# Kernel optimization log

Measured on AMD Instinct MI355X. Metric: run time of the kernel, lower is better.

Reference implementation:

```python
import jax, jax.numpy as jnp
import numpy as np

NEG_SLOPE = 0.2
NEG_INF = -1e9


def _gat_branch(x, src, dst, edge_type, t, W, a_src, a_dst, b):
    """Single-head PyG GATConv restricted (by masking) to edges with edge_type == t,
    with self-loops added (PyG default add_self_loops=True)."""
    N = x.shape[0]
    h = x @ W                                   # [N, out_dim]
    s = h @ a_src                               # [N] source attention term
    d = h @ a_dst                               # [N] destination attention term
    # real edges (masked by type)
    e_edge = jax.nn.leaky_relu(s[src] + d[dst], NEG_SLOPE)
    e_edge = jnp.where(edge_type == t, e_edge, NEG_INF)
    # self-loop edges i -> i
    e_self = jax.nn.leaky_relu(s + d, NEG_SLOPE)
    dst_all = jnp.concatenate([dst, jnp.arange(N)])          # [E+N]
    e_all = jnp.concatenate([e_edge, e_self])                 # [E+N]
    # softmax over incoming edges per destination node (segment softmax)
    m = jax.ops.segment_max(e_all, dst_all, num_segments=N)
    p = jnp.exp(e_all - m[dst_all])
    denom = jax.ops.segment_sum(p, dst_all, num_segments=N)
    alpha = p / denom[dst_all]                                 # [E+N]
    msg = jnp.concatenate([h[src], h], axis=0) * alpha[:, None]
    return jax.ops.segment_sum(msg, dst_all, num_segments=N) + b


def setup_inputs() -> dict:
    key = jax.random.key(0)
    ks = jax.random.split(key, 12)
    N, E, in_dim, out_dim = 100000, 1000000, 64, 64
    glorot = (6.0 / (in_dim + out_dim)) ** 0.5
    att = (6.0 / (1 + out_dim)) ** 0.5
    return {
        "x": jax.random.normal(ks[0], (N, in_dim), dtype=jnp.float32),
        "edge_index": jax.random.randint(ks[1], (2, E), 0, N),
        "edge_type": jax.random.randint(ks[2], (E,), 0, 2),
        "W_login": jax.random.uniform(ks[3], (in_dim, out_dim), jnp.float32, -glorot, glorot),
        "a_src_login": jax.random.uniform(ks[4], (out_dim,), jnp.float32, -att, att),
        "a_dst_login": jax.random.uniform(ks[5], (out_dim,), jnp.float32, -att, att),
        "b_login": jnp.zeros((out_dim,), jnp.float32),
        "W_exec": jax.random.uniform(ks[6], (in_dim, out_dim), jnp.float32, -glorot, glorot),
        "a_src_exec": jax.random.uniform(ks[7], (out_dim,), jnp.float32, -att, att),
        "a_dst_exec": jax.random.uniform(ks[8], (out_dim,), jnp.float32, -att, att),
        "b_exec": jnp.zeros((out_dim,), jnp.float32),
    }


def reference(x, edge_index, edge_type, W_login, a_src_login, a_dst_login, b_login,
              W_exec, a_src_exec, a_dst_exec, b_exec):
    src, dst = edge_index[0], edge_index[1]
    out = _gat_branch(x, src, dst, edge_type, 0, W_login, a_src_login, a_dst_login, b_login)
    out = out + _gat_branch(x, src, dst, edge_type, 1, W_exec, a_src_exec, a_dst_exec, b_exec)
    return out
```

## Files before the change

### kernel.cpp

```cpp
#include <hip/hip_runtime.h>

#define D 64
#define CAP 896
#define NSEG 64

typedef unsigned short u16;
typedef __attribute__((ext_vector_type(8))) __bf16 bf16x8;
typedef __attribute__((ext_vector_type(4))) float f32x4;

__device__ __forceinline__ float lrelu(float x) { return x > 0.f ? x : 0.2f * x; }
__device__ __forceinline__ u16 f2bf(float f) {
    unsigned u = __float_as_uint(f);
    return (u16)((u + 0x7fffu + ((u >> 16) & 1u)) >> 16);
}
__device__ __forceinline__ float bf2f(u16 v) { return __uint_as_float((unsigned)v << 16); }
__device__ __forceinline__ unsigned pack2(float lo, float hi) {
    return (unsigned)f2bf(lo) | ((unsigned)f2bf(hi) << 16);
}

__global__ __launch_bounds__(256) void k_gemm3(
    const float* __restrict__ x,
    const float* __restrict__ W0, const float* __restrict__ as0, const float* __restrict__ ad0,
    const float* __restrict__ W1, const float* __restrict__ as1, const float* __restrict__ ad1,
    u16* __restrict__ hb, float* __restrict__ s_tab, float* __restrict__ d_tab,
    int* __restrict__ bktcnt, int nbk, int N, int ntiles)
{
    __shared__ u16 Wb[2][64][64];
    __shared__ u16 Xb[64][72];
    __shared__ float wsd[4][64];

    const int tid = threadIdx.x;
    if (blockIdx.x == 0)
        for (int i = tid; i < nbk; i += 256) bktcnt[i] = 0;

    for (int i = tid; i < 4096; i += 256) {
        const int k = i >> 6, n = i & 63;
        Wb[0][n][k] = f2bf(W0[i]);
        Wb[1][n][k] = f2bf(W1[i]);
    }
    if (tid < 64) {
        const int k = tid;
        float q0 = 0.f, q1 = 0.f, q2 = 0.f, q3 = 0.f;
        for (int n = 0; n < 64; ++n) {
            const float w0v = W0[(k << 6) + n], w1v = W1[(k << 6) + n];
            q0 = fmaf(w0v, as0[n], q0);
            q1 = fmaf(w0v, ad0[n], q1);
            q2 = fmaf(w1v, as1[n], q2);
            q3 = fmaf(w1v, ad1[n], q3);
        }
        wsd[0][k] = q0; wsd[1][k] = q1; wsd[2][k] = q2; wsd[3][k] = q3;
    }
    __syncthreads();

    const int lane = tid & 63;
    const int nl = lane & 15, quad = lane >> 4;
    const int wv = tid >> 6;

    bf16x8 bfrag[2][4][2];
#pragma unroll
    for (int br = 0; br < 2; ++br)
#pragma unroll
        for (int t = 0; t < 4; ++t)
#pragma unroll
            for (int h = 0; h < 2; ++h)
                bfrag[br][t][h] = *(const bf16x8*)&Wb[br][t * 16 + nl][h * 32 + quad * 8];

    const int rstage = tid >> 2;
    const int kc = (tid & 3) << 4;

    for (int tile = blockIdx.x; tile < ntiles; tile += gridDim.x) {
        const long n0 = (long)tile << 6;
        __syncthreads();
        {
            long row = n0 + rstage; if (row >= N) row = N - 1;
            const float4* xp = (const float4*)(x + row * D + kc);
            const float4 v0 = xp[0], v1 = xp[1], v2 = xp[2], v3 = xp[3];

            unsigned q[8];
            q[0] = pack2(v0.x, v0.y); q[1] = pack2(v0.z, v0.w);
            q[2] = pack2(v1.x, v1.y); q[3] = pack2(v1.z, v1.w);
            q[4] = pack2(v2.x, v2.y); q[5] = pack2(v2.z, v2.w);
            q[6] = pack2(v3.x, v3.y); q[7] = pack2(v3.z, v3.w);
            *(uint4*)&Xb[rstage][kc]     = make_uint4(q[0], q[1], q[2], q[3]);
            *(uint4*)&Xb[rstage][kc + 8] = make_uint4(q[4], q[5], q[6], q[7]);

            float ps[4];
#pragma unroll
            for (int v = 0; v < 4; ++v) {
                const float4* wp = (const float4*)&wsd[v][kc];
                const float4 wa = wp[0], wb = wp[1], wc = wp[2], wd = wp[3];
                float s = 0.f;
                s = fmaf(v0.x, wa.x, s); s = fmaf(v0.y, wa.y, s);
                s = fmaf(v0.z, wa.z, s); s = fmaf(v0.w, wa.w, s);
                s = fmaf(v1.x, wb.x, s); s = fmaf(v1.y, wb.y, s);
                s = fmaf(v1.z, wb.z, s); s = fmaf(v1.w, wb.w, s);
                s = fmaf(v2.x, wc.x, s); s = fmaf(v2.y, wc.y, s);
                s = fmaf(v2.z, wc.z, s); s = fmaf(v2.w, wc.w, s);
                s = fmaf(v3.x, wd.x, s); s = fmaf(v3.y, wd.y, s);
                s = fmaf(v3.z, wd.z, s); s = fmaf(v3.w, wd.w, s);
                ps[v] = s;
            }
#pragma unroll
            for (int v = 0; v < 4; ++v) {
                ps[v] += __shfl_xor(ps[v], 1, 64);
                ps[v] += __shfl_xor(ps[v], 2, 64);
            }
            const long rw = n0 + rstage;
            if ((tid & 3) == 0 && rw < N) {
                s_tab[(rw << 1)]     = ps[0]; d_tab[(rw << 1)]     = ps[1];
                s_tab[(rw << 1) | 1] = ps[2]; d_tab[(rw << 1) | 1] = ps[3];
            }
        }
        __syncthreads();

        const int rbase = wv << 4;
        const bf16x8 a0 = *(const bf16x8*)&Xb[rbase + nl][quad * 8];
        const bf16x8 a1 = *(const bf16x8*)&Xb[rbase + nl][32 + quad * 8];

        f32x4 acc[2][4];
#pragma unroll
        for (int br = 0; br < 2; ++br)
#pragma unroll
            for (int t = 0; t < 4; ++t) {
                f32x4 c = {0.f, 0.f, 0.f, 0.f};
                c = __builtin_amdgcn_mfma_f32_16x16x32_bf16(a0, bfrag[br][t][0], c, 0, 0, 0);
                c = __builtin_amdgcn_mfma_f32_16x16x32_bf16(a1, bfrag[br][t][1], c, 0, 0, 0);
                acc[br][t] = c;
            }

#pragma unroll
        for (int reg = 0; reg < 4; ++reg) {
            const long row = n0 + rbase + (quad << 2) + reg;
            if (row < N) {
#pragma unroll
                for (int br = 0; br < 2; ++br) {
                    u16* dp = hb + (((row << 1) | br) << 6) + nl;
                    dp[0]  = f2bf(acc[br][0][reg]);
                    dp[16] = f2bf(acc[br][1][reg]);
                    dp[32] = f2bf(acc[br][2][reg]);
                    dp[48] = f2bf(acc[br][3][reg]);
                }
            }
        }
    }
}

__global__ __launch_bounds__(256) void k_bin(
    const int* __restrict__ src, const int* __restrict__ dst,
    const int* __restrict__ et, int* __restrict__ bktcnt,
    unsigned* __restrict__ bkt, int E, int nbk, int rbk, int Eseg)
{
    extern __shared__ int cnt_l[];
    const int tid = threadIdx.x;
    const int r = blockIdx.x & 7;
    const int s = blockIdx.x >> 3;
    const int lo_b = r * rbk;
    const int hi_b = min(lo_b + rbk, nbk);
    const int nb = hi_b - lo_b;
    if (nb <= 0) return;

    for (int i = tid; i < nb; i += 256) cnt_l[i] = 0;
    __syncthreads();

    const long e0 = (long)s * Eseg;
    const long e1 = min(e0 + (long)Eseg, (long)E);

    long i = e0 + tid;
    for (; i + 256 * 7 < e1; i += 256 * 8) {
        int d[8];
#pragma unroll
        for (int k = 0; k < 8; ++k) d[k] = dst[i + 256 * k];
#pragma unroll
        for (int k = 0; k < 8; ++k) {
            const int bb = d[k] >> 6;
            if (bb >= lo_b && bb < hi_b) atomicAdd(&cnt_l[bb - lo_b], 1);
        }
    }
    for (; i < e1; i += 256) {
        const int bb = dst[i] >> 6;
        if (bb >= lo_b && bb < hi_b) atomicAdd(&cnt_l[bb - lo_b], 1);
    }
    __syncthreads();

    for (int j = tid; j < nb; j += 256) {
        const int c = cnt_l[j];
        cnt_l[j] = c ? atomicAdd(bktcnt + lo_b + j, c) : 0;
    }
    __syncthreads();

    i = e0 + tid;
    for (; i + 256 * 7 < e1; i += 256 * 8) {
        int d[8];
#pragma unroll
        for (int k = 0; k < 8; ++k) d[k] = dst[i + 256 * k];
#pragma unroll
        for (int k = 0; k < 8; ++k) {
            const int bb = d[k] >> 6;
            if (bb >= lo_b && bb < hi_b) {
                const long ii = i + 256 * k;
                const int slot = atomicAdd(&cnt_l[bb - lo_b], 1);
                if (slot < CAP)
                    bkt[(long)bb * CAP + slot] =
                        ((unsigned)(d[k] & 63) << 18) | ((unsigned)src[ii] << 1) | (unsigned)et[ii];
            }
        }
    }
    for (; i < e1; i += 256) {
        const int d = dst[i];
        const int bb = d >> 6;
        if (bb >= lo_b && bb < hi_b) {
            const int slot = atomicAdd(&cnt_l[bb - lo_b], 1);
            if (slot < CAP)
                bkt[(long)bb * CAP + slot] =
                    ((unsigned)(d & 63) << 18) | ((unsigned)src[i] << 1) | (unsigned)et[i];
        }
    }
}

__global__ __launch_bounds__(256) void k_proc(
    const int* __restrict__ bktcnt, const unsigned* __restrict__ bkt,
    const float* __restrict__ s_tab, const float* __restrict__ d_tab,
    const u16* __restrict__ hb,
    const float* __restrict__ b0, const float* __restrict__ b1,
    float* __restrict__ out, int N)
{
    __shared__ unsigned tok[CAP];
    __shared__ int degl[64];
    __shared__ int curl[64];

    const int tid = threadIdx.x;
    const int b = blockIdx.x;
    const int lo = b << 6;
    const int cnt_nodes = min(64, N - lo);
    const int nb = min(bktcnt[b], CAP);

    if (tid < 64) degl[tid] = 0;
    __syncthreads();

    unsigned pr[4];
    int ns = 0;
    for (int i = tid; i < nb; i += 256) {
        const unsigned p = bkt[(long)b * CAP + i];
        pr[ns++] = p;
        atomicAdd(&degl[(p >> 18) & 63], 1);
    }
    __syncthreads();
    if (tid < 64) {
        int v = degl[tid];
        const int orig = v;
#pragma unroll
        for (int o = 1; o < 64; o <<= 1) {
            const int u = __shfl_up(v, o, 64);
            if (tid >= o) v += u;
        }
        curl[tid] = v - orig;
    }
    __syncthreads();
    for (int k = 0, i = tid; k < ns; i += 256, ++k) {
        const unsigned p = pr[k];
        const int s = atomicAdd(&curl[(p >> 18) & 63], 1);
        tok[s] = p & 0x3FFFFu;
    }
    __syncthreads();

    const int lane = tid & 63;
    const int wave = tid >> 6;

    for (int ni = wave; ni < cnt_nodes; ni += 4) {
        const int n = lo + ni;
        const int deg = degl[ni];
        const int off = curl[ni] - deg;
        const float d0n = d_tab[(n << 1)];
        const float d1n = d_tab[(n << 1) | 1];

        if (deg <= 62) {
            const int cnt = deg + 2;
            unsigned cmb = 0; unsigned t = 0; float e = 0.f;
            if (lane < deg) {
                cmb = tok[off + lane];
                t = cmb & 1u;
                e = lrelu(s_tab[cmb] + (t ? d1n : d0n));
            } else if (lane == deg)   { cmb = (unsigned)(n << 1);      t = 0; e = lrelu(s_tab[cmb] + d0n); }
            else if (lane == deg + 1) { cmb = (unsigned)(n << 1) | 1u; t = 1; e = lrelu(s_tab[cmb] + d1n); }

            const bool act = lane < cnt;
            const float p = act ? __expf(e) : 0.f;
            float p0 = t ? 0.f : p;
            float p1 = t ? p : 0.f;
#pragma unroll
            for (int o = 32; o; o >>= 1) {
                p0 += __shfl_xor(p0, o, 64);
                p1 += __shfl_xor(p1, o, 64);
            }
            const float a_r = act ? p / (t ? p1 : p0) : 0.f;

            const int colb = (lane & 31) << 1;
            const int half = lane >> 5;
            float2 acc = {0.f, 0.f};
            const int np = (cnt + 1) >> 1;
            int pp = 0;
            for (; pp + 1 < np; pp += 2) {
                const int iA = (pp << 1) + half;
                const int iB = iA + 2;
                const int iBc = iB < cnt ? iB : cnt - 1;
                float aA    = __shfl(a_r, iA, 64);
                unsigned cA = __shfl(cmb, iA, 64);
                float aB    = __shfl(a_r, iBc, 64);
                unsigned cB = __shfl(cmb, iBc, 64);
                if (iB >= cnt) aB = 0.f;
                const unsigned uA = *(const unsigned*)(hb + ((long)cA << 6) + colb);
                const unsigned uB = *(const unsigned*)(hb + ((long)cB << 6) + colb);
                acc.x = fmaf(aA, __uint_as_float(uA << 16), acc.x);
                acc.y = fmaf(aA, __uint_as_float(uA & 0xffff0000u), acc.y);
                acc.x = fmaf(aB, __uint_as_float(uB << 16), acc.x);
                acc.y = fmaf(aB, __uint_as_float(uB & 0xffff0000u), acc.y);
            }
            if (pp < np) {
                const int iA = (pp << 1) + half;
                const int iAc = iA < cnt ? iA : cnt - 1;
                float aA    = __shfl(a_r, iAc, 64);
                unsigned cA = __shfl(cmb, iAc, 64);
                if (iA >= cnt) aA = 0.f;
                const unsigned uA = *(const unsigned*)(hb + ((long)cA << 6) + colb);
                acc.x = fmaf(aA, __uint_as_float(uA << 16), acc.x);
                acc.y = fmaf(aA, __uint_as_float(uA & 0xffff0000u), acc.y);
            }
            acc.x += __shfl_xor(acc.x, 32, 64);
            acc.y += __shfl_xor(acc.y, 32, 64);
            if (lane < 32) {
                float2 o;
                o.x = acc.x + b0[colb] + b1[colb];
                o.y = acc.y + b0[colb + 1] + b1[colb + 1];
                *(float2*)(out + ((long)n << 6) + colb) = o;
            }
        } else {
            const float es0 = lrelu(s_tab[(n << 1)] + d0n);
            const float es1 = lrelu(s_tab[(n << 1) | 1] + d1n);
            float p0 = 0.f, p1 = 0.f;
            for (int j = lane; j < deg; j += 64) {
                const unsigned c = tok[off + j];
                const float e = lrelu(s_tab[c] + ((c & 1u) ? d1n : d0n));
                if (c & 1u) p1 += __expf(e); else p0 += __expf(e);
            }
#pragma unroll
            for (int o = 32; o; o >>= 1) {
                p0 += __shfl_xor(p0, o, 64);
                p1 += __shfl_xor(p1, o, 64);
            }
            const float den0 = p0 + __expf(es0);
            const float den1 = p1 + __expf(es1);

            float acc = (__expf(es0) / den0) * bf2f(hb[((long)n << 7) + lane])
                      + (__expf(es1) / den1) * bf2f(hb[((long)n << 7) + 64 + lane]);
            for (int base = 0; base < deg; base += 64) {
                const int j = base + lane;
                unsigned ck = 0; float a = 0.f;
                if (j < deg) {
                    ck = tok[off + j];
                    const float e = lrelu(s_tab[ck] + ((ck & 1u) ? d1n : d0n));
                    a = __expf(e) / ((ck & 1u) ? den1 : den0);
                }
                const int lim = min(64, deg - base);
                for (int jj = 0; jj < lim; ++jj) {
                    const float aj = __shfl(a, jj, 64);
                    const unsigned cj = __shfl(ck, jj, 64);
                    acc = fmaf(aj, bf2f(hb[((long)cj << 6) + lane]), acc);
                }
            }
            out[((long)n << 6) + lane] = acc + b0[lane] + b1[lane];
        }
    }
}

extern "C" void kernel_launch(void* const* d_in, const int* in_sizes, int n_in,
                              void* d_out, int out_size, void* d_ws, size_t ws_size,
                              hipStream_t stream) {
    const float* x   = (const float*)d_in[0];
    const int*   ei  = (const int*)d_in[1];
    const int*   et  = (const int*)d_in[2];
    const float* W0  = (const float*)d_in[3];
    const float* as0 = (const float*)d_in[4];
    const float* ad0 = (const float*)d_in[5];
    const float* b0  = (const float*)d_in[6];
    const float* W1  = (const float*)d_in[7];
    const float* as1 = (const float*)d_in[8];
    const float* ad1 = (const float*)d_in[9];
    const float* b1  = (const float*)d_in[10];
    float* out = (float*)d_out;

    const int N = in_sizes[0] / D;
    const int E = in_sizes[1] / 2;
    const int* src = ei;
    const int* dst = ei + E;

    const int nbk = (N + 63) >> 6;

    char* w = (char*)d_ws;
    u16* hb = (u16*)w;            w += (size_t)2 * N * D * sizeof(u16);
    float* s_tab = (float*)w;     w += (size_t)2 * N * sizeof(float);
    float* d_tab = (float*)w;     w += (size_t)2 * N * sizeof(float);
    int* bktcnt = (int*)w;        w += (size_t)nbk * sizeof(int);
    unsigned* bkt = (unsigned*)w; w += (size_t)nbk * CAP * sizeof(unsigned);

    const int ntiles = (N + 63) / 64;
    const int rbk = (nbk + 7) / 8;
    const int Eseg = (E + NSEG - 1) / NSEG;

    k_gemm3<<<768, 256, 0, stream>>>(x, W0, as0, ad0, W1, as1, ad1,
                                     hb, s_tab, d_tab, bktcnt, nbk, N, ntiles);
    k_bin<<<8 * NSEG, 256, (size_t)rbk * sizeof(int), stream>>>(
        src, dst, et, bktcnt, bkt, E, nbk, rbk, Eseg);
    k_proc<<<nbk, 256, 0, stream>>>(bktcnt, bkt, s_tab, d_tab, hb, b0, b1, out, N);
}
```

Baseline: 211.7 us.

## Bin edges in single pass over all buckets and widen gather loads

Replaces the range-partitioned binning kernel (8 bucket ranges × 64 segments) with one kernel of 64 blocks, each counting and scattering over all buckets. This removes the repeated reads of dst across bucket ranges but leaves only 64 blocks, far fewer than the GPU's compute units. The per-node gather now has each lane load 4 bf16 features (8 bytes) and handles 4 edges per wave step, with an extra shuffle reduction. The attention-vector precompute is also spread over all four waves.

After: 205.0 us. 1.03x faster.

```diff
diff --git a/kernel.cpp b/kernel.cpp
--- a/kernel.cpp
+++ b/kernel.cpp
@@ -2,7 +2,7 @@
 
 #define D 64
 #define CAP 896
-#define NSEG 64
+#define BINB 64
 
 typedef unsigned short u16;
 typedef __attribute__((ext_vector_type(8))) __bf16 bf16x8;
@@ -17,6 +17,8 @@
 __device__ __forceinline__ unsigned pack2(float lo, float hi) {
     return (unsigned)f2bf(lo) | ((unsigned)f2bf(hi) << 16);
 }
+__device__ __forceinline__ float blo(unsigned u) { return __uint_as_float(u << 16); }
+__device__ __forceinline__ float bhi(unsigned u) { return __uint_as_float(u & 0xffff0000u); }
 
 __global__ __launch_bounds__(256) void k_gemm3(
     const float* __restrict__ x,
@@ -38,17 +40,14 @@
         Wb[0][n][k] = f2bf(W0[i]);
         Wb[1][n][k] = f2bf(W1[i]);
     }
-    if (tid < 64) {
-        const int k = tid;
-        float q0 = 0.f, q1 = 0.f, q2 = 0.f, q3 = 0.f;
-        for (int n = 0; n < 64; ++n) {
-            const float w0v = W0[(k << 6) + n], w1v = W1[(k << 6) + n];
-            q0 = fmaf(w0v, as0[n], q0);
-            q1 = fmaf(w0v, ad0[n], q1);
-            q2 = fmaf(w1v, as1[n], q2);
-            q3 = fmaf(w1v, ad1[n], q3);
-        }
-        wsd[0][k] = q0; wsd[1][k] = q1; wsd[2][k] = q2; wsd[3][k] = q3;
+    {
+        const int k = tid & 63;
+        const int v = tid >> 6;
+        const float* Ws = (v < 2) ? W0 : W1;
+        const float* av = (v == 0) ? as0 : (v == 1) ? ad0 : (v == 2) ? as1 : ad1;
+        float q = 0.f;
+        for (int n = 0; n < 64; ++n) q = fmaf(Ws[(k << 6) + n], av[n], q);
+        wsd[v][k] = q;
     }
     __syncthreads();
 
@@ -145,24 +144,17 @@
     }
 }
 
-__global__ __launch_bounds__(256) void k_bin(
+__global__ __launch_bounds__(256) void k_bin1(
     const int* __restrict__ src, const int* __restrict__ dst,
     const int* __restrict__ et, int* __restrict__ bktcnt,
-    unsigned* __restrict__ bkt, int E, int nbk, int rbk, int Eseg)
+    unsigned* __restrict__ bkt, int E, int nbk, int Eseg)
 {
     extern __shared__ int cnt_l[];
     const int tid = threadIdx.x;
-    const int r = blockIdx.x & 7;
-    const int s = blockIdx.x >> 3;
-    const int lo_b = r * rbk;
-    const int hi_b = min(lo_b + rbk, nbk);
-    const int nb = hi_b - lo_b;
-    if (nb <= 0) return;
-
-    for (int i = tid; i < nb; i += 256) cnt_l[i] = 0;
-    __syncthreads();
-
-    const long e0 = (long)s * Eseg;
+    for (int i = tid; i < nbk; i += 256) cnt_l[i] = 0;
+    __syncthreads();
+
+    const long e0 = (long)blockIdx.x * Eseg;
     const long e1 = min(e0 + (long)Eseg, (long)E);
 
     long i = e0 + tid;
@@ -171,20 +163,14 @@
 #pragma unroll
         for (int k = 0; k < 8; ++k) d[k] = dst[i + 256 * k];
 #pragma unroll
-        for (int k = 0; k < 8; ++k) {
-            const int bb = d[k] >> 6;
-            if (bb >= lo_b && bb < hi_b) atomicAdd(&cnt_l[bb - lo_b], 1);
-        }
-    }
-    for (; i < e1; i += 256) {
-        const int bb = dst[i] >> 6;
-        if (bb >= lo_b && bb < hi_b) atomicAdd(&cnt_l[bb - lo_b], 1);
-    }
-    __syncthreads();
-
-    for (int j = tid; j < nb; j += 256) {
+        for (int k = 0; k < 8; ++k) atomicAdd(&cnt_l[d[k] >> 6], 1);
+    }
+    for (; i < e1; i += 256) atomicAdd(&cnt_l[dst[i] >> 6], 1);
+    __syncthreads();
+
+    for (int j = tid; j < nbk; j += 256) {
         const int c = cnt_l[j];
-        cnt_l[j] = c ? atomicAdd(bktcnt + lo_b + j, c) : 0;
+        cnt_l[j] = c ? atomicAdd(bktcnt + j, c) : 0;
     }
     __syncthreads();
 
@@ -196,24 +182,20 @@
 #pragma unroll
         for (int k = 0; k < 8; ++k) {
             const int bb = d[k] >> 6;
-            if (bb >= lo_b && bb < hi_b) {
-                const long ii = i + 256 * k;
-                const int slot = atomicAdd(&cnt_l[bb - lo_b], 1);
-                if (slot < CAP)
-                    bkt[(long)bb * CAP + slot] =
-                        ((unsigned)(d[k] & 63) << 18) | ((unsigned)src[ii] << 1) | (unsigned)et[ii];
-            }
+            const long ii = i + 256 * k;
+            const int slot = atomicAdd(&cnt_l[bb], 1);
+            if (slot < CAP)
+                bkt[(long)bb * CAP + slot] =
+                    ((unsigned)(d[k] & 63) << 18) | ((unsigned)src[ii] << 1) | (unsigned)et[ii];
         }
     }
     for (; i < e1; i += 256) {
         const int d = dst[i];
         const int bb = d >> 6;
-        if (bb >= lo_b && bb < hi_b) {
-            const int slot = atomicAdd(&cnt_l[bb - lo_b], 1);
-            if (slot < CAP)
-                bkt[(long)bb * CAP + slot] =
-                    ((unsigned)(d & 63) << 18) | ((unsigned)src[i] << 1) | (unsigned)et[i];
-        }
+        const int slot = atomicAdd(&cnt_l[bb], 1);
+        if (slot < CAP)
+            bkt[(long)bb * CAP + slot] =
+                ((unsigned)(d & 63) << 18) | ((unsigned)src[i] << 1) | (unsigned)et[i];
     }
 }
 
@@ -265,6 +247,8 @@
 
     const int lane = tid & 63;
     const int wave = tid >> 6;
+    const int q = lane >> 4;
+    const int cl = lane & 15;
 
     for (int ni = wave; ni < cnt_nodes; ni += 4) {
         const int n = lo + ni;
@@ -294,44 +278,57 @@
             }
             const float a_r = act ? p / (t ? p1 : p0) : 0.f;
 
-            const int colb = (lane & 31) << 1;
-            const int half = lane >> 5;
-            float2 acc = {0.f, 0.f};
-            const int np = (cnt + 1) >> 1;
+            float4 acc = {0.f, 0.f, 0.f, 0.f};
+            const int nq = (cnt + 3) >> 2;
             int pp = 0;
-            for (; pp + 1 < np; pp += 2) {
-                const int iA = (pp << 1) + half;
-                const int iB = iA + 2;
+            for (; pp + 1 < nq; pp += 2) {
+                const int iA = (pp << 2) + q;
+                const int iB = iA + 4;
                 const int iBc = iB < cnt ? iB : cnt - 1;
                 float aA    = __shfl(a_r, iA, 64);
                 unsigned cA = __shfl(cmb, iA, 64);
                 float aB    = __shfl(a_r, iBc, 64);
                 unsigned cB = __shfl(cmb, iBc, 64);
                 if (iB >= cnt) aB = 0.f;
-                const unsigned uA = *(const unsigned*)(hb + ((long)cA << 6) + colb);
-                const unsigned uB = *(const unsigned*)(hb + ((long)cB << 6) + colb);
-                acc.x = fmaf(aA, __uint_as_float(uA << 16), acc.x);
-                acc.y = fmaf(aA, __uint_as_float(uA & 0xffff0000u), acc.y);
-                acc.x = fmaf(aB, __uint_as_float(uB << 16), acc.x);
-                acc.y = fmaf(aB, __uint_as_float(uB & 0xffff0000u), acc.y);
-            }
-            if (pp < np) {
-                const int iA = (pp << 1) + half;
+                const uint2 uA = *(const uint2*)(hb + ((long)cA << 6) + (cl << 2));
+                const uint2 uB = *(const uint2*)(hb + ((long)cB << 6) + (cl << 2));
+                acc.x = fmaf(aA, blo(uA.x), acc.x);
+                acc.y = fmaf(aA, bhi(uA.x), acc.y);
+                acc.z = fmaf(aA, blo(uA.y), acc.z);
+                acc.w = fmaf(aA, bhi(uA.y), acc.w);
+                acc.x = fmaf(aB, blo(uB.x), acc.x);
+                acc.y = fmaf(aB, bhi(uB.x), acc.y);
+                acc.z = fmaf(aB, blo(uB.y), acc.z);
+                acc.w = fmaf(aB, bhi(uB.y), acc.w);
+            }
+            if (pp < nq) {
+                const int iA = (pp << 2) + q;
                 const int iAc = iA < cnt ? iA : cnt - 1;
                 float aA    = __shfl(a_r, iAc, 64);
                 unsigned cA = __shfl(cmb, iAc, 64);
                 if (iA >= cnt) aA = 0.f;
-                const unsigned uA = *(const unsigned*)(hb + ((long)cA << 6) + colb);
-                acc.x = fmaf(aA, __uint_as_float(uA << 16), acc.x);
-                acc.y = fmaf(aA, __uint_as_float(uA & 0xffff0000u), acc.y);
-            }
+                const uint2 uA = *(const uint2*)(hb + ((long)cA << 6) + (cl << 2));
+                acc.x = fmaf(aA, blo(uA.x), acc.x);
+                acc.y = fmaf(aA, bhi(uA.x), acc.y);
+                acc.z = fmaf(aA, blo(uA.y), acc.z);
+                acc.w = fmaf(aA, bhi(uA.y), acc.w);
+            }
+            acc.x += __shfl_xor(acc.x, 16, 64);
+            acc.y += __shfl_xor(acc.y, 16, 64);
+            acc.z += __shfl_xor(acc.z, 16, 64);
+            acc.w += __shfl_xor(acc.w, 16, 64);
             acc.x += __shfl_xor(acc.x, 32, 64);
             acc.y += __shfl_xor(acc.y, 32, 64);
-            if (lane < 32) {
-                float2 o;
-                o.x = acc.x + b0[colb] + b1[colb];
-                o.y = acc.y + b0[colb + 1] + b1[colb + 1];
-                *(float2*)(out + ((long)n << 6) + colb) = o;
+            acc.z += __shfl_xor(acc.z, 32, 64);
+            acc.w += __shfl_xor(acc.w, 32, 64);
+            if (lane < 16) {
+                const int c0 = cl << 2;
+                float4 o;
+                o.x = acc.x + b0[c0]     + b1[c0];
+                o.y = acc.y + b0[c0 + 1] + b1[c0 + 1];
+                o.z = acc.z + b0[c0 + 2] + b1[c0 + 2];
+                o.w = acc.w + b0[c0 + 3] + b1[c0 + 3];
+                *(float4*)(out + ((long)n << 6) + c0) = o;
             }
         } else {
             const float es0 = lrelu(s_tab[(n << 1)] + d0n);
@@ -403,12 +400,11 @@
     unsigned* bkt = (unsigned*)w; w += (size_t)nbk * CAP * sizeof(unsigned);
 
     const int ntiles = (N + 63) / 64;
-    const int rbk = (nbk + 7) / 8;
-    const int Eseg = (E + NSEG - 1) / NSEG;
+    const int Eseg = (E + BINB - 1) / BINB;
 
     k_gemm3<<<768, 256, 0, stream>>>(x, W0, as0, ad0, W1, as1, ad1,
                                      hb, s_tab, d_tab, bktcnt, nbk, N, ntiles);
-    k_bin<<<8 * NSEG, 256, (size_t)rbk * sizeof(int), stream>>>(
-        src, dst, et, bktcnt, bkt, E, nbk, rbk, Eseg);
+    k_bin1<<<BINB, 256, (size_t)nbk * sizeof(int), stream>>>(
+        src, dst, et, bktcnt, bkt, E, nbk, Eseg);
     k_proc<<<nbk, 256, 0, stream>>>(bktcnt, bkt, s_tab, d_tab, hb, b0, b1, out, N);
 }
```
